# Kernel tuning notes

Hardware: AMD Instinct MI355X
Metric: run time of the kernel (lower is better)

Reference implementation:

```python
import jax, jax.numpy as jnp
import numpy as np

B, S, D, H, HD, TOPK = 2, 2048, 2048, 16, 128, 256
HIDDEN = 4 * D
EPS = 1e-6


def setup_inputs() -> dict:
    key = jax.random.key(0)
    ks = jax.random.split(key, 12)
    def g(k, shape, scale):
        return jax.random.normal(k, shape, dtype=jnp.float32) * scale
    # rotary tables: freqs_cis[s, i] = (cos, sin) of s * theta_i
    theta = 1.0 / (10000.0 ** (np.arange(0, HD, 2, dtype=np.float32) / HD))  # [HD/2]
    ang = np.arange(S, dtype=np.float32)[:, None] * theta[None, :]           # [S, HD/2]
    freqs_cis = jnp.asarray(np.stack([np.cos(ang), np.sin(ang)], axis=-1))   # [S, HD/2, 2]
    return {
        "x": g(ks[0], (B, S, D), 1.0),
        "start_pos": 0,
        "freqs_cis": freqs_cis,
        "router_w": g(ks[1], (D, 1), D ** -0.5),
        "wq": g(ks[2], (D, H * HD), D ** -0.5),
        "wk": g(ks[3], (D, H * HD), D ** -0.5),
        "wv": g(ks[4], (D, H * HD), D ** -0.5),
        "wo": g(ks[5], (H * HD, D), (H * HD) ** -0.5),
        "w1": g(ks[6], (D, HIDDEN), D ** -0.5),
        "w2": g(ks[7], (HIDDEN, D), HIDDEN ** -0.5),
        "w3": g(ks[8], (D, HIDDEN), D ** -0.5),
        "attn_norm_w": jnp.ones((D,), jnp.float32),
        "ffn_norm_w": jnp.ones((D,), jnp.float32),
    }


def _rmsnorm(x, w, eps=EPS):
    return x * jax.lax.rsqrt(jnp.mean(x * x, axis=-1, keepdims=True) + eps) * w


def _rotary(q, freqs):  # q: [B,S,H,HD], freqs: [S,HD/2,2]
    q = q.reshape(*q.shape[:-1], HD // 2, 2)
    cos = freqs[None, :, None, :, 0]
    sin = freqs[None, :, None, :, 1]
    qr = q[..., 0] * cos - q[..., 1] * sin
    qi = q[..., 0] * sin + q[..., 1] * cos
    return jnp.stack([qr, qi], axis=-1).reshape(*q.shape[:-2], HD)


def _attention(xn, freqs, tok_mask, wq, wk, wv, wo):
    b, s, _ = xn.shape
    q = (xn @ wq).reshape(b, s, H, HD)
    k = (xn @ wk).reshape(b, s, H, HD)
    v = (xn @ wv).reshape(b, s, H, HD)
    q = _rotary(q, freqs)
    k = _rotary(k, freqs)
    scores = jnp.einsum("bqhd,bkhd->bhqk", q, k) / np.sqrt(HD).astype(np.float32)
    # keys of non-selected tokens are masked out (MoD routing mask)
    scores = scores + jnp.where(tok_mask[:, None, None, :] > 0, 0.0, -1e9)
    attn = jax.nn.softmax(scores, axis=-1)
    out = jnp.einsum("bhqk,bkhd->bqhd", attn, v).reshape(b, s, H * HD)
    return out @ wo


def reference(x, start_pos, freqs_cis, router_w, wq, wk, wv, wo, w1, w2, w3, attn_norm_w, ffn_norm_w):
    b, s, _ = x.shape
    freqs = jax.lax.dynamic_slice_in_dim(freqs_cis, start_pos, s, axis=0)
    # --- router: top-k token selection + scatter mask ---
    token_weights = x @ router_w                      # [B,S,1]
    topk_vals, topk_idx = jax.lax.top_k(token_weights[..., 0], TOPK)
    mask = jnp.zeros((b, s), x.dtype).at[jnp.arange(b)[:, None], topk_idx].set(1.0)
    masked_input = x * mask[:, :, None]
    # --- dense attention + FFN on masked tokens ---
    h = masked_input + _attention(_rmsnorm(masked_input, attn_norm_w), freqs, mask, wq, wk, wv, wo)
    hn = _rmsnorm(h, ffn_norm_w)
    out = (jax.nn.silu(hn @ w1) * (hn @ w3)) @ w2    # SwiGLU FFN
    return out, token_weights, topk_idx
```

## Files before the change

### kernel.cpp

```cpp
#include <hip/hip_runtime.h>
#include <hip/hip_bf16.h>
#include <math.h>

#define B_ 2
#define S_ 2048
#define D_ 2048
#define H_ 16
#define HD_ 128
#define TOPK_ 256
#define HIDDEN_ 8192
#define EPS_ 1e-6f

constexpr int ROWS_SEL = B_ * TOPK_;
constexpr int ROWS_ALL = ROWS_SEL + B_;

typedef __attribute__((ext_vector_type(8))) short bf16x8;
typedef __attribute__((ext_vector_type(4))) float f32x4;

__device__ __forceinline__ short f2bf(float f) {
    __hip_bfloat16 h = __float2bfloat16(f);
    return *reinterpret_cast<short*>(&h);
}

__device__ __forceinline__ float bf2f(short s) {
    union { unsigned u; float f; } c;
    c.u = ((unsigned)(unsigned short)s) << 16;
    return c.f;
}

__device__ __forceinline__ void gll16(const void* g, void* l) {
    __builtin_amdgcn_global_load_lds(
        (const __attribute__((address_space(1))) unsigned int*)g,
        (__attribute__((address_space(3))) unsigned int*)l, 16, 0, 0);
}

__device__ __forceinline__ float block_sum_256(float v, float* red4) {
    for (int o = 32; o; o >>= 1) v += __shfl_down(v, o);
    if ((threadIdx.x & 63) == 0) red4[threadIdx.x >> 6] = v;
    __syncthreads();
    float t = red4[0] + red4[1] + red4[2] + red4[3];
    __syncthreads();
    return t;
}

__device__ __forceinline__ float block_max_256(float v, float* red4) {
    for (int o = 32; o; o >>= 1) v = fmaxf(v, __shfl_down(v, o));
    if ((threadIdx.x & 63) == 0) red4[threadIdx.x >> 6] = v;
    __syncthreads();
    float t = fmaxf(fmaxf(red4[0], red4[1]), fmaxf(red4[2], red4[3]));
    __syncthreads();
    return t;
}

__global__ __launch_bounds__(256) void router_kernel(const float* __restrict__ x,
                                                     const float* __restrict__ rw,
                                                     float* __restrict__ tw) {
    int token = blockIdx.x;
    const float4* xr = (const float4*)(x + (long)token * D_);
    const float4* r4 = (const float4*)rw;
    float s = 0.f;
    for (int c = threadIdx.x; c < D_ / 4; c += 256) {
        float4 a = xr[c], b = r4[c];
        s += a.x * b.x + a.y * b.y + a.z * b.z + a.w * b.w;
    }
    __shared__ float red4[4];
    float tot = block_sum_256(s, red4);
    if (threadIdx.x == 0) tw[token] = tot;
}

__global__ __launch_bounds__(1024) void topk_kernel(const float* __restrict__ tw,
                                                    float* __restrict__ idx_out,
                                                    int* __restrict__ sel_idx,
                                                    int* __restrict__ sel_pos) {
    int b = blockIdx.x;
    __shared__ float v[S_];
    __shared__ int id[S_];
    int t = threadIdx.x;
    for (int i = t; i < S_; i += 1024) {
        v[i] = tw[b * S_ + i];
        id[i] = i;
        sel_pos[b * S_ + i] = -1;
    }
    __syncthreads();
    for (int k = 2; k <= S_; k <<= 1) {
        for (int j = k >> 1; j > 0; j >>= 1) {
            for (int i = t; i < S_; i += 1024) {
                int ixj = i ^ j;
                if (ixj > i) {
                    float va = v[i], vb = v[ixj];
                    int ia = id[i], ib = id[ixj];
                    bool before = (va > vb) || (va == vb && ia < ib);
                    bool dir = ((i & k) == 0);
                    if (dir != before) {
                        v[i] = vb; v[ixj] = va;
                        id[i] = ib; id[ixj] = ia;
                    }
                }
            }
            __syncthreads();
        }
    }
    if (t < TOPK_) {
        idx_out[b * TOPK_ + t] = (float)id[t];
        sel_idx[b * TOPK_ + t] = id[t];
        sel_pos[b * S_ + id[t]] = t;
    }
}

__global__ __launch_bounds__(256) void gather_rmsnorm_kernel(const float* __restrict__ x,
                                                             const int* __restrict__ sel_idx,
                                                             const float* __restrict__ nw,
                                                             short* __restrict__ XN) {
    int r = blockIdx.x;
    int b = r >> 8;
    int s = sel_idx[r];
    const float* xr = x + ((long)b * S_ + s) * D_;
    __shared__ float buf[D_];
    __shared__ float red4[4];
    float ss = 0.f;
    for (int c = threadIdx.x; c < D_; c += 256) {
        float vv = xr[c];
        buf[c] = vv;
        ss += vv * vv;
    }
    float tot = block_sum_256(ss, red4);
    float scale = rsqrtf(tot / D_ + EPS_);
    for (int c = threadIdx.x; c < D_; c += 256)
        XN[(long)r * D_ + c] = f2bf(buf[c] * scale * nw[c]);
}

__global__ __launch_bounds__(256) void gemm_mfma_w(
    const short* __restrict__ A,
    const float* __restrict__ B0, const float* __restrict__ B1, const float* __restrict__ B2,
    float* __restrict__ Cb, long czStride, long spStride,
    int M, int N, int Ktot, int K_per, int splits) {
    __shared__ short As[128 * 32];
    __shared__ short Bs[128 * 32];
    int z = blockIdx.z;
    int zmat = z / splits, sp = z % splits;
    const float* Bm = (zmat == 0) ? B0 : (zmat == 1) ? B1 : B2;
    float* C = Cb + (long)zmat * czStride + (long)sp * spStride;
    int kbase = sp * K_per;
    int row0 = blockIdx.y * 128, col0 = blockIdx.x * 128;
    int t = threadIdx.x;
    int lane = t & 63, w = t >> 6;
    int l16 = lane & 15, quad = lane >> 4;
    int wr = (w >> 1) * 64, wc = (w & 1) * 64;
    int arr = t >> 2, ach = (t & 3) * 8;
    int bn = t & 127, bkh = (t >> 7) * 16;
    int bswz = (bn >> 1) & 3;
    short* bw0 = Bs + bn * 32 + ((((bkh >> 3) + 0) ^ bswz) << 3);
    short* bw1 = Bs + bn * 32 + ((((bkh >> 3) + 1) ^ bswz) << 3);
    const float* bcol = Bm + col0 + bn;
    f32x4 acc[4][4] = {};
    for (int k0 = kbase; k0 < kbase + K_per; k0 += 32) {
        __syncthreads();
        #pragma unroll
        for (int rd = 0; rd < 2; ++rd) {
            int ar = row0 + arr + rd * 64; ar = (ar < M) ? ar : (M - 1);
            gll16(A + (size_t)ar * Ktot + k0 + ach, (char*)As + rd * 4096 + t * 16);
        }
        const float* src = bcol + (size_t)(k0 + bkh) * N;
        float f[16];
        #pragma unroll
        for (int r = 0; r < 16; ++r) f[r] = src[(size_t)r * N];
        union { short s[8]; bf16x8 v; } u0, u1;
        #pragma unroll
        for (int r = 0; r < 8; ++r) u0.s[r] = f2bf(f[r]);
        #pragma unroll
        for (int r = 0; r < 8; ++r) u1.s[r] = f2bf(f[r + 8]);
        *(bf16x8*)bw0 = u0.v;
        *(bf16x8*)bw1 = u1.v;
        __syncthreads();
        bf16x8 af[4], bfr[4];
        #pragma unroll
        for (int i = 0; i < 4; ++i)
            af[i] = *(const bf16x8*)(As + (wr + i * 16 + l16) * 32 + quad * 8);
        #pragma unroll
        for (int j = 0; j < 4; ++j) {
            int n = wc + j * 16 + l16;
            bfr[j] = *(const bf16x8*)(Bs + n * 32 + ((quad ^ ((n >> 1) & 3)) << 3));
        }
        #pragma unroll
        for (int i = 0; i < 4; ++i)
            #pragma unroll
            for (int j = 0; j < 4; ++j)
                acc[i][j] = __builtin_amdgcn_mfma_f32_16x16x32_bf16(af[i], bfr[j], acc[i][j], 0, 0, 0);
    }
    #pragma unroll
    for (int i = 0; i < 4; ++i) {
        #pragma unroll
        for (int r = 0; r < 4; ++r) {
            int row = row0 + wr + i * 16 + quad * 4 + r;
            if (row < M) {
                #pragma unroll
                for (int j = 0; j < 4; ++j)
                    C[(size_t)row * N + col0 + wc + j * 16 + l16] = acc[i][j][r];
            }
        }
    }
}

template <bool OBF>
__global__ __launch_bounds__(256) void gemm_mfma_attn(
    const short* __restrict__ A, long sAo, long sAi, int lda,
    const short* __restrict__ Bm, long sBo, long sBi, int ldb,
    void* __restrict__ Cv, long sCo, long sCi, int ldc,
    int M, int N, int K, int inner) {
    __shared__ short smem[2 * 128 * 32];
    short* As = smem;
    short* Bs = smem + 128 * 32;
    int z = blockIdx.z;
    int zo = z / inner, zi = z % inner;
    const short* Ab = A + (long)zo * sAo + (long)zi * sAi;
    const short* Bb = Bm + (long)zo * sBo + (long)zi * sBi;
    long cbase = (long)zo * sCo + (long)zi * sCi;
    int row0 = blockIdx.y * 128, col0 = blockIdx.x * 128;
    int t = threadIdx.x;
    int lane = t & 63, w = t >> 6;
    int l16 = lane & 15, quad = lane >> 4;
    int wr = (w >> 1) * 64, wc = (w & 1) * 64;
    int rr = t >> 2, ch = (t & 3) * 8;
    f32x4 acc[4][4] = {};
    for (int k0 = 0; k0 < K; k0 += 32) {
        __syncthreads();
        #pragma unroll
        for (int rd = 0; rd < 2; ++rd) {
            int r = rr + rd * 64;
            int ar = row0 + r; ar = (ar < M) ? ar : (M - 1);
            gll16(Ab + (size_t)ar * lda + k0 + ch, (char*)As + rd * 4096 + t * 16);
            gll16(Bb + (size_t)(col0 + r) * ldb + k0 + ch, (char*)Bs + rd * 4096 + t * 16);
        }
        __syncthreads();
        bf16x8 af[4], bfr[4];
        #pragma unroll
        for (int i = 0; i < 4; ++i)
            af[i] = *(const bf16x8*)(As + (wr + i * 16 + l16) * 32 + quad * 8);
        #pragma unroll
        for (int j = 0; j < 4; ++j)
            bfr[j] = *(const bf16x8*)(Bs + (wc + j * 16 + l16) * 32 + quad * 8);
        #pragma unroll
        for (int i = 0; i < 4; ++i)
            #pragma unroll
            for (int j = 0; j < 4; ++j)
                acc[i][j] = __builtin_amdgcn_mfma_f32_16x16x32_bf16(af[i], bfr[j], acc[i][j], 0, 0, 0);
    }
    #pragma unroll
    for (int i = 0; i < 4; ++i) {
        #pragma unroll
        for (int r = 0; r < 4; ++r) {
            int row = row0 + wr + i * 16 + quad * 4 + r;
            if (row < M) {
                #pragma unroll
                for (int j = 0; j < 4; ++j) {
                    long idx = cbase + (size_t)row * ldc + col0 + wc + j * 16 + l16;
                    if (OBF) ((short*)Cv)[idx] = f2bf(acc[i][j][r]);
                    else     ((float*)Cv)[idx] = acc[i][j][r];
                }
            }
        }
    }
}

__global__ __launch_bounds__(256) void qkv_finish(
    const float* __restrict__ Cp, const float* __restrict__ fc,
    const int* __restrict__ sel_idx, const int* __restrict__ sp0,
    short* __restrict__ Qbf, short* __restrict__ Kbf, short* __restrict__ Vbf,
    int splits) {
    int r = blockIdx.x;
    int s = sel_idx[r];
    int pos = sp0[0] + s;
    const float* f = fc + (long)pos * HD_;
    const long matS = (long)ROWS_SEL * D_;
    const long spS = 3 * matS;
    const float* qp = Cp + (long)r * D_;
    const float* kp = qp + matS;
    const float* vp = qp + 2 * matS;
    const float qscale = 0.08838834764831845f;
    for (int p = threadIdx.x; p < (D_ / 2); p += 256) {
        int h = p >> 6, d2 = p & 63;
        int e0 = h * HD_ + d2 * 2;
        float q0 = 0.f, q1 = 0.f, k0 = 0.f, k1 = 0.f, v0 = 0.f, v1 = 0.f;
        for (int sp = 0; sp < splits; ++sp) {
            long off = (long)sp * spS;
            q0 += qp[off + e0]; q1 += qp[off + e0 + 1];
            k0 += kp[off + e0]; k1 += kp[off + e0 + 1];
            v0 += vp[off + e0]; v1 += vp[off + e0 + 1];
        }
        float c = f[d2 * 2], sn = f[d2 * 2 + 1];
        Qbf[(long)r * D_ + e0]     = f2bf((q0 * c - q1 * sn) * qscale);
        Qbf[(long)r * D_ + e0 + 1] = f2bf((q0 * sn + q1 * c) * qscale);
        Kbf[(long)r * D_ + e0]     = f2bf(k0 * c - k1 * sn);
        Kbf[(long)r * D_ + e0 + 1] = f2bf(k0 * sn + k1 * c);
        Vbf[(long)r * D_ + e0]     = f2bf(v0);
        Vbf[(long)r * D_ + e0 + 1] = f2bf(v1);
    }
}

__global__ __launch_bounds__(256) void vt_kernel(const short* __restrict__ Vbf,
                                                 short* __restrict__ VT) {
    int z = blockIdx.z;
    int b = z >> 4, h = z & 15;
    int key0 = blockIdx.x * 64, d0 = blockIdx.y * 64;
    __shared__ short L[64][72];
    int t = threadIdx.x;
    int kr = t >> 3, dc = (t & 7) * 8;
    #pragma unroll
    for (int rr = 0; rr < 2; ++rr) {
        int key = kr + rr * 32;
        union { short s[8]; int4 v; } u;
        u.v = *(const int4*)&Vbf[(size_t)(b * 256 + key0 + key) * D_ + h * 128 + d0 + dc];
        #pragma unroll
        for (int j = 0; j < 8; ++j) L[key][dc + j] = u.s[j];
    }
    __syncthreads();
    int dr = t >> 3, kc = (t & 7) * 8;
    #pragma unroll
    for (int rr = 0; rr < 2; ++rr) {
        int d = dr + rr * 32;
        union { short s[8]; int4 v; } u;
        #pragma unroll
        for (int j = 0; j < 8; ++j) u.s[j] = L[kc + j][d];
        *(int4*)&VT[((size_t)z * 128 + d0 + d) * 256 + key0 + kc] = u.v;
    }
}

__global__ __launch_bounds__(256) void softmax_kernel(const float* __restrict__ SC,
                                                      short* __restrict__ Pbf) {
    long row = blockIdx.x;
    const float* p = SC + row * 256;
    int t = threadIdx.x;
    float v = p[t];
    __shared__ float red4[4];
    float m = block_max_256(v, red4);
    float e = expf(v - m);
    float s = block_sum_256(e, red4);
    Pbf[row * 256 + t] = f2bf(e / s);
}

__global__ __launch_bounds__(256) void vbar_kernel(const short* __restrict__ Vbf,
                                                   short* __restrict__ Obf) {
    int b = blockIdx.y;
    int c = blockIdx.x * 256 + threadIdx.x;
    float s = 0.f;
    for (int i = 0; i < TOPK_; ++i) s += bf2f(Vbf[((long)b * TOPK_ + i) * D_ + c]);
    Obf[(long)(ROWS_SEL + b) * D_ + c] = f2bf(s * (1.f / TOPK_));
}

__global__ __launch_bounds__(256) void resid_rmsnorm_kernel(const float* __restrict__ Pp,
                                                            int splits,
                                                            const float* __restrict__ x,
                                                            const int* __restrict__ sel_idx,
                                                            const float* __restrict__ nw,
                                                            short* __restrict__ HN) {
    int r = blockIdx.x;
    __shared__ float buf[D_];
    __shared__ float red4[4];
    const long spS = (long)ROWS_ALL * D_;
    const float* pr = Pp + (long)r * D_;
    const float* xr = nullptr;
    if (r < ROWS_SEL) {
        int b = r >> 8;
        int s = sel_idx[r];
        xr = x + ((long)b * S_ + s) * D_;
    }
    float ss = 0.f;
    for (int c = threadIdx.x; c < D_; c += 256) {
        float v = xr ? xr[c] : 0.f;
        for (int sp = 0; sp < splits; ++sp) v += pr[(long)sp * spS + c];
        buf[c] = v;
        ss += v * v;
    }
    float tot = block_sum_256(ss, red4);
    float scale = rsqrtf(tot / D_ + EPS_);
    for (int c = threadIdx.x; c < D_; c += 256)
        HN[(long)r * D_ + c] = f2bf(buf[c] * scale * nw[c]);
}

__global__ __launch_bounds__(256) void reduce_silu_kernel(const float* __restrict__ Gp,
                                                          short* __restrict__ FF, long n) {
    long i = (long)blockIdx.x * 256 + threadIdx.x;
    if (i < n) {
        const long cz = (long)ROWS_ALL * HIDDEN_;
        float a = Gp[i] + Gp[cz + i];
        float g = Gp[2 * cz + i] + Gp[3 * cz + i];
        FF[i] = f2bf((a / (1.f + expf(-a))) * g);
    }
}

__global__ __launch_bounds__(256) void w2_reduce_kernel(const float* __restrict__ Wp,
                                                        float* __restrict__ OUTR, long n4) {
    long i = (long)blockIdx.x * 256 + threadIdx.x;
    if (i < n4) {
        const long spS4 = (long)ROWS_ALL * D_ / 4;
        float4 s = ((const float4*)Wp)[i];
        for (int sp = 1; sp < 8; ++sp) {
            float4 v = ((const float4*)Wp)[(long)sp * spS4 + i];
            s.x += v.x; s.y += v.y; s.z += v.z; s.w += v.w;
        }
        ((float4*)OUTR)[i] = s;
    }
}

__global__ __launch_bounds__(256) void scatter_kernel(const float* __restrict__ OUTR,
                                                      const int* __restrict__ sel_pos,
                                                      float* __restrict__ out) {
    int blk = blockIdx.x;
    int b = blk >> 11;
    int p = sel_pos[blk];
    int row = (p >= 0) ? (b * TOPK_ + p) : (ROWS_SEL + b);
    const float4* src = (const float4*)(OUTR + (long)row * D_);
    float4* dst = (float4*)(out + (long)blk * D_);
    for (int c = threadIdx.x; c < D_ / 4; c += 256) dst[c] = src[c];
}

extern "C" void kernel_launch(void* const* d_in, const int* in_sizes, int n_in,
                              void* d_out, int out_size, void* d_ws, size_t ws_size,
                              hipStream_t stream) {
    const float* x        = (const float*)d_in[0];
    const int*   startpos = (const int*)d_in[1];
    const float* freqs    = (const float*)d_in[2];
    const float* router_w = (const float*)d_in[3];
    const float* wq       = (const float*)d_in[4];
    const float* wk       = (const float*)d_in[5];
    const float* wv       = (const float*)d_in[6];
    const float* wo       = (const float*)d_in[7];
    const float* w1       = (const float*)d_in[8];
    const float* w2       = (const float*)d_in[9];
    const float* w3       = (const float*)d_in[10];
    const float* attn_w   = (const float*)d_in[11];
    const float* ffn_w    = (const float*)d_in[12];

    float* out     = (float*)d_out;
    float* tw_out  = out + (long)B_ * S_ * D_;
    float* idx_out = tw_out + (long)B_ * S_;

    char* ws = (char*)d_ws;
    auto alloc = [&](size_t bytes) -> void* {
        void* p = (void*)ws;
        ws += (bytes + 255) / 256 * 256;
        return p;
    };
    int*   sel_idx = (int*)alloc((size_t)B_ * TOPK_ * sizeof(int));
    int*   sel_pos = (int*)alloc((size_t)B_ * S_ * sizeof(int));
    short* XNbf = (short*)alloc((size_t)ROWS_SEL * D_ * sizeof(short));
    short* Qbf  = (short*)alloc((size_t)ROWS_SEL * D_ * sizeof(short));
    short* Kbf  = (short*)alloc((size_t)ROWS_SEL * D_ * sizeof(short));
    short* Vbf  = (short*)alloc((size_t)ROWS_SEL * D_ * sizeof(short));
    short* VT   = (short*)alloc((size_t)B_ * H_ * HD_ * TOPK_ * sizeof(short));
    float* SC   = (float*)alloc((size_t)B_ * H_ * TOPK_ * TOPK_ * sizeof(float));
    short* Pbf  = (short*)alloc((size_t)B_ * H_ * TOPK_ * TOPK_ * sizeof(short));
    short* Obf  = (short*)alloc((size_t)ROWS_ALL * D_ * sizeof(short));
    short* HNbf = (short*)alloc((size_t)ROWS_ALL * D_ * sizeof(short));
    short* FFbf = (short*)alloc((size_t)ROWS_ALL * HIDDEN_ * sizeof(short));
    float* OUTR = (float*)alloc((size_t)ROWS_ALL * D_ * sizeof(float));
    float* Gar  = (float*)alloc((size_t)4 * ROWS_ALL * HIDDEN_ * sizeof(float));

    router_kernel<<<B_ * S_, 256, 0, stream>>>(x, router_w, tw_out);
    topk_kernel<<<B_, 1024, 0, stream>>>(tw_out, idx_out, sel_idx, sel_pos);
    gather_rmsnorm_kernel<<<ROWS_SEL, 256, 0, stream>>>(x, sel_idx, attn_w, XNbf);
    {
        dim3 g(D_ / 128, ROWS_SEL / 128, 3 * 4);
        gemm_mfma_w<<<g, 256, 0, stream>>>(XNbf, wq, wk, wv,
                                           Gar, (long)ROWS_SEL * D_, (long)3 * ROWS_SEL * D_,
                                           ROWS_SEL, D_, D_, D_ / 4, 4);
    }
    qkv_finish<<<ROWS_SEL, 256, 0, stream>>>(Gar, freqs, sel_idx, startpos, Qbf, Kbf, Vbf, 4);
    {
        dim3 g(4, 2, B_ * H_);
        vt_kernel<<<g, 256, 0, stream>>>(Vbf, VT);
    }
    {
        dim3 g(2, 2, B_ * H_);
        gemm_mfma_attn<false><<<g, 256, 0, stream>>>(
            Qbf, (long)TOPK_ * D_, HD_, D_,
            Kbf, (long)TOPK_ * D_, HD_, D_,
            SC, (long)H_ * TOPK_ * TOPK_, (long)TOPK_ * TOPK_, TOPK_,
            TOPK_, TOPK_, HD_, H_);
    }
    softmax_kernel<<<B_ * H_ * TOPK_, 256, 0, stream>>>(SC, Pbf);
    {
        dim3 g(1, 2, B_ * H_);
        gemm_mfma_attn<true><<<g, 256, 0, stream>>>(
            Pbf, (long)H_ * TOPK_ * TOPK_, (long)TOPK_ * TOPK_, TOPK_,
            VT, (long)H_ * HD_ * TOPK_, (long)HD_ * TOPK_, TOPK_,
            Obf, (long)TOPK_ * D_, HD_, D_,
            TOPK_, HD_, TOPK_, H_);
    }
    {
        dim3 g(D_ / 256, B_, 1);
        vbar_kernel<<<g, 256, 0, stream>>>(Vbf, Obf);
    }
    {
        dim3 g(D_ / 128, (ROWS_ALL + 127) / 128, 8);
        gemm_mfma_w<<<g, 256, 0, stream>>>(Obf, wo, wo, wo,
                                           Gar, 0, (long)ROWS_ALL * D_,
                                           ROWS_ALL, D_, D_, D_ / 8, 8);
    }
    resid_rmsnorm_kernel<<<ROWS_ALL, 256, 0, stream>>>(Gar, 8, x, sel_idx, ffn_w, HNbf);
    {
        dim3 g(HIDDEN_ / 128, (ROWS_ALL + 127) / 128, 2 * 2);
        gemm_mfma_w<<<g, 256, 0, stream>>>(HNbf, w1, w3, w3,
                                           Gar, (long)2 * ROWS_ALL * HIDDEN_, (long)ROWS_ALL * HIDDEN_,
                                           ROWS_ALL, HIDDEN_, D_, D_ / 2, 2);
    }
    {
        long n = (long)ROWS_ALL * HIDDEN_;
        reduce_silu_kernel<<<(unsigned)((n + 255) / 256), 256, 0, stream>>>(Gar, FFbf, n);
    }
    {
        dim3 g(D_ / 128, (ROWS_ALL + 127) / 128, 8);
        gemm_mfma_w<<<g, 256, 0, stream>>>(FFbf, w2, w2, w2,
                                           Gar, 0, (long)ROWS_ALL * D_,
                                           ROWS_ALL, D_, HIDDEN_, HIDDEN_ / 8, 8);
    }
    {
        long n4 = (long)ROWS_ALL * D_ / 4;
        w2_reduce_kernel<<<(unsigned)((n4 + 255) / 256), 256, 0, stream>>>(Gar, OUTR, n4);
    }
    scatter_kernel<<<B_ * S_, 256, 0, stream>>>(OUTR, sel_pos, out);
}
```

Measured before the change: 564.4 us.

## Double-buffer LDS in weight GEMM and prefetch next K tile into registers

Converts gemm_mfma_w's As/Bs shared tiles into two buffers and software-pipelines the K loop. While the MFMAs run on the current tile, the next tile's fp32 weight loads go to registers and the A tile is fetched into the other buffer with direct global-to-LDS loads. Explicit vmcnt waits and sched barriers control the ordering. This aims to hide global memory latency behind compute, at the cost of double the LDS and fragile hand-counted waitcnt values.

```diff
diff --git a/kernel.cpp b/kernel.cpp
--- a/kernel.cpp
+++ b/kernel.cpp
@@ -134,8 +134,8 @@
     const float* __restrict__ B0, const float* __restrict__ B1, const float* __restrict__ B2,
     float* __restrict__ Cb, long czStride, long spStride,
     int M, int N, int Ktot, int K_per, int splits) {
-    __shared__ short As[128 * 32];
-    __shared__ short Bs[128 * 32];
+    __shared__ short As[2][128 * 32];
+    __shared__ short Bs[2][128 * 32];
     int z = blockIdx.z;
     int zmat = z / splits, sp = z % splits;
     const float* Bm = (zmat == 0) ? B0 : (zmat == 1) ? B1 : B2;
@@ -149,43 +149,70 @@
     int arr = t >> 2, ach = (t & 3) * 8;
     int bn = t & 127, bkh = (t >> 7) * 16;
     int bswz = (bn >> 1) & 3;
-    short* bw0 = Bs + bn * 32 + ((((bkh >> 3) + 0) ^ bswz) << 3);
-    short* bw1 = Bs + bn * 32 + ((((bkh >> 3) + 1) ^ bswz) << 3);
+    int bw0o = bn * 32 + ((((bkh >> 3) + 0) ^ bswz) << 3);
+    int bw1o = bn * 32 + ((((bkh >> 3) + 1) ^ bswz) << 3);
     const float* bcol = Bm + col0 + bn;
+    int ar0 = row0 + arr;      ar0 = (ar0 < M) ? ar0 : (M - 1);
+    int ar1 = row0 + arr + 64; ar1 = (ar1 < M) ? ar1 : (M - 1);
+    const short* Ap0 = A + (size_t)ar0 * Ktot + ach;
+    const short* Ap1 = A + (size_t)ar1 * Ktot + ach;
+
     f32x4 acc[4][4] = {};
-    for (int k0 = kbase; k0 < kbase + K_per; k0 += 32) {
-        __syncthreads();
-        #pragma unroll
-        for (int rd = 0; rd < 2; ++rd) {
-            int ar = row0 + arr + rd * 64; ar = (ar < M) ? ar : (M - 1);
-            gll16(A + (size_t)ar * Ktot + k0 + ach, (char*)As + rd * 4096 + t * 16);
-        }
-        const float* src = bcol + (size_t)(k0 + bkh) * N;
-        float f[16];
+    float f[16];
+
+    {
+        const float* src = bcol + (size_t)(kbase + bkh) * N;
         #pragma unroll
         for (int r = 0; r < 16; ++r) f[r] = src[(size_t)r * N];
+        gll16(Ap0 + kbase, (char*)As[0] + t * 16);
+        gll16(Ap1 + kbase, (char*)As[0] + 4096 + t * 16);
+    }
+
+    int nk = K_per >> 5;
+    for (int kt = 0; kt < nk; ++kt) {
+        int cur = kt & 1;
+        short* Bsc = Bs[cur];
+        asm volatile("s_waitcnt vmcnt(2)" ::: "memory");
+        __builtin_amdgcn_sched_barrier(0);
         union { short s[8]; bf16x8 v; } u0, u1;
         #pragma unroll
         for (int r = 0; r < 8; ++r) u0.s[r] = f2bf(f[r]);
         #pragma unroll
         for (int r = 0; r < 8; ++r) u1.s[r] = f2bf(f[r + 8]);
-        *(bf16x8*)bw0 = u0.v;
-        *(bf16x8*)bw1 = u1.v;
-        __syncthreads();
+        *(bf16x8*)(Bsc + bw0o) = u0.v;
+        *(bf16x8*)(Bsc + bw1o) = u1.v;
+        if (kt + 1 < nk) {
+            int k1 = kbase + (kt + 1) * 32;
+            const float* src = bcol + (size_t)(k1 + bkh) * N;
+            #pragma unroll
+            for (int r = 0; r < 16; ++r) f[r] = src[(size_t)r * N];
+            char* Adst = (char*)As[cur ^ 1];
+            gll16(Ap0 + k1, Adst + t * 16);
+            gll16(Ap1 + k1, Adst + 4096 + t * 16);
+            asm volatile("s_waitcnt vmcnt(18) lgkmcnt(0)" ::: "memory");
+        } else {
+            asm volatile("s_waitcnt vmcnt(0) lgkmcnt(0)" ::: "memory");
+        }
+        __builtin_amdgcn_sched_barrier(0);
+        __builtin_amdgcn_s_barrier();
+        __builtin_amdgcn_sched_barrier(0);
+        const short* Asc = As[cur];
         bf16x8 af[4], bfr[4];
         #pragma unroll
         for (int i = 0; i < 4; ++i)
-            af[i] = *(const bf16x8*)(As + (wr + i * 16 + l16) * 32 + quad * 8);
+            af[i] = *(const bf16x8*)(Asc + (wr + i * 16 + l16) * 32 + quad * 8);
         #pragma unroll
         for (int j = 0; j < 4; ++j) {
             int n = wc + j * 16 + l16;
-            bfr[j] = *(const bf16x8*)(Bs + n * 32 + ((quad ^ ((n >> 1) & 3)) << 3));
+            bfr[j] = *(const bf16x8*)(Bsc + n * 32 + ((quad ^ ((n >> 1) & 3)) << 3));
         }
         #pragma unroll
         for (int i = 0; i < 4; ++i)
             #pragma unroll
             for (int j = 0; j < 4; ++j)
                 acc[i][j] = __builtin_amdgcn_mfma_f32_16x16x32_bf16(af[i], bfr[j], acc[i][j], 0, 0, 0);
+        __builtin_amdgcn_s_barrier();
+        __builtin_amdgcn_sched_barrier(0);
     }
     #pragma unroll
     for (int i = 0; i < 4; ++i) {
```

Result: no change. 559.0 us (-1.0%).
